# Optimization experiments

Measured on AMD Instinct MI355X. Metric: run time of the kernel, lower is better.

Reference implementation:

```python
import jax, jax.numpy as jnp
import numpy as np

D_MODEL, D_STATE, D_CONV, EXPAND = 1024, 16, 4, 2
D_INNER = EXPAND * D_MODEL
BATCH, SEQ = 2, 2048


def setup_inputs() -> dict:
    key = jax.random.key(0)
    ks = jax.random.split(key, 10)
    inv = lambda n: 1.0 / np.sqrt(n)
    return {
        "x": jax.random.normal(ks[0], (BATCH, SEQ, D_MODEL), jnp.float32),
        "in_proj_w": jax.random.uniform(ks[1], (2 * D_INNER, D_MODEL), jnp.float32, -inv(D_MODEL), inv(D_MODEL)),
        "conv_w": jax.random.uniform(ks[2], (D_INNER, D_INNER, D_CONV), jnp.float32, -inv(D_INNER * D_CONV), inv(D_INNER * D_CONV)),
        "conv_b": jax.random.uniform(ks[3], (D_INNER,), jnp.float32, -inv(D_INNER * D_CONV), inv(D_INNER * D_CONV)),
        "dt_w": jax.random.uniform(ks[4], (D_INNER, D_INNER), jnp.float32, -inv(D_INNER), inv(D_INNER)),
        "dt_b": jax.random.uniform(ks[5], (D_INNER,), jnp.float32, -inv(D_INNER), inv(D_INNER)),
        "A_log": jax.random.normal(ks[6], (D_INNER, D_STATE), jnp.float32) * 0.01,
        "D": jnp.ones((D_INNER,), jnp.float32),
        "B_w": jax.random.uniform(ks[7], (D_STATE, D_INNER), jnp.float32, -inv(D_INNER), inv(D_INNER)),
        "C_w": jax.random.uniform(ks[8], (D_STATE, D_INNER), jnp.float32, -inv(D_INNER), inv(D_INNER)),
        "out_w": jax.random.uniform(ks[9], (D_MODEL, D_INNER), jnp.float32, -inv(D_INNER), inv(D_INNER)),
    }


def _forward(x, in_proj_w, conv_w, conv_b, dt_w, dt_b, A_log, D, B_w, C_w, out_w):
    xz = x @ in_proj_w.T                      # [b, l, 2*d_inner]
    xc, z = jnp.split(xz, 2, axis=-1)
    # causal depthful conv1d (full channel mixing, left-padded)
    h = jnp.transpose(xc, (0, 2, 1))          # [b, d, l]
    h = jnp.pad(h, ((0, 0), (0, 0), (D_CONV - 1, 0)))
    h = jax.lax.conv_general_dilated(h, conv_w, (1,), 'VALID',
                                     dimension_numbers=('NCH', 'OIH', 'NCH'))
    h = h + conv_b[None, :, None]
    u = jnp.transpose(h, (0, 2, 1))           # [b, l, d_inner]

    dt = jnp.clip(jax.nn.sigmoid(u @ dt_w.T + dt_b), 1e-4, 1.0)  # [b, l, d]
    A = -jnp.exp(A_log)                       # [d, n]
    Bm = u @ B_w.T                            # [b, l, n]
    Cm = u @ C_w.T                            # [b, l, n]

    # time-major scan over the recurrence
    u_t = jnp.transpose(u, (1, 0, 2))
    dt_t = jnp.transpose(dt, (1, 0, 2))
    B_t = jnp.transpose(Bm, (1, 0, 2))
    C_t = jnp.transpose(Cm, (1, 0, 2))

    def step(state, inp):
        ut, dtt, bt, ct = inp                 # [b,d], [b,d], [b,n], [b,n]
        dA = jnp.exp(jnp.clip(dtt[:, :, None] * A, -5.0, 5.0))   # [b,d,n]
        dB = dtt[:, :, None] * bt[:, None, :] * ut[:, :, None]   # [b,d,n]
        state = dA * state + dB + 1e-6
        y = jnp.sum(state * ct[:, None, :], axis=-1) + D * ut    # [b,d]
        return state, y

    state0 = jnp.zeros((x.shape[0], D_INNER, D_STATE), x.dtype)
    _, ys = jax.lax.scan(step, state0, (u_t, dt_t, B_t, C_t))
    y = jnp.transpose(ys, (1, 0, 2))          # [b, l, d_inner]
    y = y * jax.nn.silu(z)
    return y @ out_w.T                        # [b, l, d_model]


def reference(x, in_proj_w, conv_w, conv_b, dt_w, dt_b, A_log, D, B_w, C_w, out_w):
    return _forward(x, in_proj_w, conv_w, conv_b, dt_w, dt_b, A_log, D, B_w, C_w, out_w)
```

## Files before the change

kernel.cpp:

```cpp
#include <hip/hip_runtime.h>

#define BATCHN 2
#define SEQL   2048
#define DM     1024
#define DI     2048
#define DSN    16
#define MTOT   (BATCHN * SEQL)
#define PADL   (SEQL + 3)
#define NC     64
#define CL     (SEQL / NC)
#define BCKS   8

typedef __attribute__((ext_vector_type(8))) __bf16 bf16x8;
typedef __attribute__((ext_vector_type(4))) float f32x4;

__device__ __forceinline__ unsigned short f2b(float f) {
    union { float f; unsigned u; } v; v.f = f;
    unsigned r = v.u + 0x7FFF + ((v.u >> 16) & 1);
    return (unsigned short)(r >> 16);
}
__device__ __forceinline__ float b2f(unsigned short b) {
    union { float f; unsigned u; } v; v.u = ((unsigned)b) << 16;
    return v.f;
}

__device__ __forceinline__ void gl_lds16(const void* g, void* l) {
    __builtin_amdgcn_global_load_lds(
        (const __attribute__((address_space(1))) unsigned int*)g,
        (__attribute__((address_space(3))) unsigned int*)l, 16, 0, 0);
}

__device__ __forceinline__ void swz(int& bx, int& by) {
    int gx = gridDim.x, gy = gridDim.y;
    int lin = blockIdx.y * gx + blockIdx.x;
    int xcd = lin & 7, k = lin >> 3;
    int rw = gx >> 1, rh = gy >> 2;
    by = (xcd >> 1) * rh + k / rw;
    bx = (xcd & 1) * rw + k % rw;
}

__global__ void cvt_f32_bf16(const float* __restrict__ src, unsigned short* __restrict__ dst, int n4) {
    int i = blockIdx.x * blockDim.x + threadIdx.x;
    if (i < n4) {
        float4 v = ((const float4*)src)[i];
        ushort4 o;
        o.x = f2b(v.x); o.y = f2b(v.y); o.z = f2b(v.z); o.w = f2b(v.w);
        ((ushort4*)dst)[i] = o;
    }
}

__global__ void cvt_x_pad(const float* __restrict__ src, unsigned short* __restrict__ dst) {
    int i = blockIdx.x * blockDim.x + threadIdx.x;
    if (i < MTOT * DM / 4) {
        int b = i >> 19;
        float4 v = ((const float4*)src)[i];
        ushort4 o;
        o.x = f2b(v.x); o.y = f2b(v.y); o.z = f2b(v.z); o.w = f2b(v.w);
        ((ushort4*)dst)[i + (b + 1) * (3 * DM / 4)] = o;
    }
}

__global__ void cvt_convw(const float* __restrict__ cw, unsigned short* __restrict__ wk) {
    int i = blockIdx.x * blockDim.x + threadIdx.x;
    if (i < DI * DI) {
        float4 v = ((const float4*)cw)[i];
        wk[0 * (size_t)DI * DI + i] = f2b(v.x);
        wk[1 * (size_t)DI * DI + i] = f2b(v.y);
        wk[2 * (size_t)DI * DI + i] = f2b(v.z);
        wk[3 * (size_t)DI * DI + i] = f2b(v.w);
    }
}

__global__ void __launch_bounds__(256)
tp_cvt(const float* __restrict__ src, unsigned short* __restrict__ dst) {
    __shared__ float tile[32][33];
    int ct = blockIdx.x * 32, it = blockIdx.y * 32;
    int tx = threadIdx.x & 31, ty = threadIdx.x >> 5;
#pragma unroll
    for (int r = 0; r < 4; ++r)
        tile[ty + r * 8][tx] = src[(size_t)(it + ty + r * 8) * DM + ct + tx];
    __syncthreads();
#pragma unroll
    for (int r = 0; r < 4; ++r)
        dst[(size_t)(ct + ty + r * 8) * DI + it + tx] = f2b(tile[tx][ty + r * 8]);
}

__global__ void zero_pad(unsigned short* __restrict__ xpad) {
    int i = blockIdx.x * blockDim.x + threadIdx.x;
    if (i < BATCHN * 3 * DM) {
        int b = i / (3 * DM);
        int r = i % (3 * DM);
        xpad[(size_t)b * PADL * DM + r] = 0;
    }
}

template<int MODE>
__global__ void __launch_bounds__(256)
gemm_bt(const unsigned short* __restrict__ Abase,
        const unsigned short* __restrict__ Bbase,
        const float* __restrict__ bias,
        unsigned short* __restrict__ out_bf,
        float* __restrict__ out_f,
        int K)
{
    __shared__ __align__(16) unsigned short As[128 * 64];
    __shared__ __align__(16) unsigned short Bs[128 * 64];

    const int t = threadIdx.x;
    const int lane = t & 63;
    const int wave = t >> 6;
    const int wm = wave & 1, wn = wave >> 1;
    int bx, by;
    swz(bx, by);
    const int m0 = by * 128, n0 = bx * 128;
    const int srow = t >> 3;
    const int scol = (t & 7) * 8;
    const int gcol = (((t & 7) ^ (srow & 7))) * 8;

    f32x4 acc[4][4];
#pragma unroll
    for (int i = 0; i < 4; ++i)
#pragma unroll
        for (int j = 0; j < 4; ++j)
            acc[i][j] = f32x4{0.f, 0.f, 0.f, 0.f};

    const int nseg = (MODE == 1) ? 4 : 1;
    for (int seg = 0; seg < nseg; ++seg) {
        const unsigned short* arow[4];
        const unsigned short* brow[4];
#pragma unroll
        for (int i = 0; i < 4; ++i) {
            int rg = m0 + srow + i * 32;
            if (MODE == 0) {
                arow[i] = Abase + ((size_t)(rg >> 11) * PADL + 3 + (rg & 2047)) * DM;
            } else if (MODE == 1) {
                arow[i] = Abase + ((size_t)(rg >> 11) * PADL + (rg & 2047) + seg) * DM;
            } else if (MODE == 4) {
                arow[i] = Abase + (size_t)blockIdx.z * DI * DI + (size_t)rg * K;
            } else {
                arow[i] = Abase + (size_t)rg * K;
            }
            int ng = n0 + srow + i * 32;
            if (MODE == 1)
                brow[i] = Bbase + (size_t)seg * DI * DM + (size_t)ng * DM;
            else
                brow[i] = Bbase + (size_t)ng * K;
        }
        const int Kseg = (MODE == 1) ? DM : K;
        for (int k0 = 0; k0 < Kseg; k0 += 64) {
#pragma unroll
            for (int i = 0; i < 4; ++i)
                gl_lds16(arow[i] + k0 + gcol, &As[(size_t)(srow + i * 32) * 64 + scol]);
#pragma unroll
            for (int i = 0; i < 4; ++i)
                gl_lds16(brow[i] + k0 + gcol, &Bs[(size_t)(srow + i * 32) * 64 + scol]);
            __syncthreads();
            const int qa = (lane >> 4) * 8;
            const int am = lane & 15;
            const int sw = (am & 7) << 3;
#pragma unroll
            for (int kk = 0; kk < 64; kk += 32) {
                bf16x8 af[4], bfv[4];
#pragma unroll
                for (int i = 0; i < 4; ++i)
                    af[i] = *(const bf16x8*)&As[(wm * 64 + i * 16 + am) * 64 + ((kk + qa) ^ sw)];
#pragma unroll
                for (int j = 0; j < 4; ++j)
                    bfv[j] = *(const bf16x8*)&Bs[(wn * 64 + j * 16 + am) * 64 + ((kk + qa) ^ sw)];
#pragma unroll
                for (int i = 0; i < 4; ++i)
#pragma unroll
                    for (int j = 0; j < 4; ++j)
                        acc[i][j] = __builtin_amdgcn_mfma_f32_16x16x32_bf16(
                            af[i], bfv[j], acc[i][j], 0, 0, 0);
            }
            __syncthreads();
        }
    }

    const int erow0 = m0 + wm * 64;
    const int ecol0 = n0 + wn * 64 + (lane & 15);
    const int rq = (lane >> 4) * 4;
#pragma unroll
    for (int i = 0; i < 4; ++i) {
#pragma unroll
        for (int j = 0; j < 4; ++j) {
            int col = ecol0 + j * 16;
#pragma unroll
            for (int r = 0; r < 4; ++r) {
                int row = erow0 + i * 16 + rq + r;
                float v = acc[i][j][r];
                if (MODE == 0) {
                    out_bf[(size_t)row * DI + col] = f2b(v);
                } else if (MODE == 1) {
                    v += bias[col];
                    out_bf[(size_t)row * DI + col] = f2b(v);
                } else if (MODE == 2) {
                    v += bias[col];
                    float s = 1.f / (1.f + __expf(-v));
                    s = fminf(fmaxf(s, 1e-4f), 1.f);
                    out_f[(size_t)row * DI + col] = s;
                } else if (MODE == 3) {
                    out_f[(size_t)row * DM + col] = v;
                } else {
                    out_bf[(size_t)blockIdx.z * DI * DM + (size_t)row * DM + col] = f2b(v);
                }
            }
        }
    }
}

__global__ void __launch_bounds__(256)
bc_mfma(const unsigned short* __restrict__ u,
        const unsigned short* __restrict__ w,
        float* __restrict__ pc)
{
    const int t = threadIdx.x;
    const int lane = t & 63;
    const int wave = t >> 6;
    const int ks = blockIdx.x;
    const int m0 = blockIdx.y * 128 + wave * 32;
    const int am = lane & 15, quad = lane >> 4;

    f32x4 acc[2][2];
#pragma unroll
    for (int i = 0; i < 2; ++i)
#pragma unroll
        for (int j = 0; j < 2; ++j)
            acc[i][j] = f32x4{0.f, 0.f, 0.f, 0.f};

    const int kbase = ks * (DI / BCKS);
    const unsigned short* ur0 = u + (size_t)(m0 + am) * DI;
    const unsigned short* ur1 = u + (size_t)(m0 + 16 + am) * DI;
    const unsigned short* wr0 = w + (size_t)am * DI;
    const unsigned short* wr1 = w + (size_t)(16 + am) * DI;
#pragma unroll 2
    for (int kk = 0; kk < DI / BCKS; kk += 32) {
        int k = kbase + kk + quad * 8;
        bf16x8 a0 = *(const bf16x8*)(ur0 + k);
        bf16x8 a1 = *(const bf16x8*)(ur1 + k);
        bf16x8 b0 = *(const bf16x8*)(wr0 + k);
        bf16x8 b1 = *(const bf16x8*)(wr1 + k);
        acc[0][0] = __builtin_amdgcn_mfma_f32_16x16x32_bf16(a0, b0, acc[0][0], 0, 0, 0);
        acc[0][1] = __builtin_amdgcn_mfma_f32_16x16x32_bf16(a0, b1, acc[0][1], 0, 0, 0);
        acc[1][0] = __builtin_amdgcn_mfma_f32_16x16x32_bf16(a1, b0, acc[1][0], 0, 0, 0);
        acc[1][1] = __builtin_amdgcn_mfma_f32_16x16x32_bf16(a1, b1, acc[1][1], 0, 0, 0);
    }
    float* base = pc + (size_t)ks * MTOT * 32;
#pragma unroll
    for (int i = 0; i < 2; ++i)
#pragma unroll
        for (int j = 0; j < 2; ++j)
#pragma unroll
            for (int r = 0; r < 4; ++r) {
                int row = m0 + i * 16 + quad * 4 + r;
                int col = j * 16 + am;
                base[(size_t)row * 32 + col] = acc[i][j][r];
            }
}

__global__ void __launch_bounds__(256)
bc_reduce(const float* __restrict__ pc, float* __restrict__ outf)
{
    int i = blockIdx.x * 256 + threadIdx.x;
    const float4* p4 = (const float4*)pc;
    float4 s = p4[i];
#pragma unroll
    for (int ks = 1; ks < BCKS; ++ks) {
        float4 v = p4[(size_t)ks * (MTOT * 8) + i];
        s.x += v.x; s.y += v.y; s.z += v.z; s.w += v.w;
    }
    ((float4*)outf)[i] = s;
}

__global__ void __launch_bounds__(256)
scan_p1(const float* __restrict__ dtf,
        const unsigned short* __restrict__ u_bf,
        const float* __restrict__ bcf,
        const float* __restrict__ A_log,
        float* __restrict__ Pbuf,
        float* __restrict__ Sbuf)
{
    const int t = threadIdx.x;
    const int blk = blockIdx.x;
    const int c  = blk & (NC - 1);
    const int dh = (blk >> 6) & 7;
    const int b  = blk >> 9;
    const int d  = dh * 256 + t;

    float Adn[16];
    {
        const float4* ar = (const float4*)(A_log + (size_t)d * DSN);
#pragma unroll
        for (int q = 0; q < 4; ++q) {
            float4 v = ar[q];
            Adn[q * 4 + 0] = -__expf(v.x);
            Adn[q * 4 + 1] = -__expf(v.y);
            Adn[q * 4 + 2] = -__expf(v.z);
            Adn[q * 4 + 3] = -__expf(v.w);
        }
    }
    float s[16], P[16];
#pragma unroll
    for (int n = 0; n < 16; ++n) { s[n] = 0.f; P[n] = 1.f; }

    const size_t rowbase = (size_t)b * SEQL + (size_t)c * CL;
    for (int l0 = 0; l0 < CL; l0 += 4) {
        float dt4[4], u4[4];
#pragma unroll
        for (int j = 0; j < 4; ++j) {
            size_t rb = rowbase + l0 + j;
            dt4[j] = dtf[rb * DI + d];
            u4[j] = b2f(u_bf[rb * DI + d]);
        }
#pragma unroll
        for (int j = 0; j < 4; ++j) {
            size_t rb = rowbase + l0 + j;
            const float4* Br = (const float4*)(bcf + rb * 32);
            float Bn[16];
#pragma unroll
            for (int q = 0; q < 4; ++q) {
                float4 v = Br[q];
                Bn[q * 4 + 0] = v.x; Bn[q * 4 + 1] = v.y;
                Bn[q * 4 + 2] = v.z; Bn[q * 4 + 3] = v.w;
            }
            float dt = dt4[j];
            float dBu = dt * u4[j];
#pragma unroll
            for (int n = 0; n < 16; ++n) {
                float x = dt * Adn[n];
                x = fminf(fmaxf(x, -5.f), 5.f);
                float dA = __expf(x);
                P[n] *= dA;
                s[n] = dA * s[n] + (dBu * Bn[n] + 1e-6f);
            }
        }
    }
    size_t ob = (((size_t)c * BATCHN + b) * DI + d) * DSN;
#pragma unroll
    for (int q = 0; q < 4; ++q) {
        ((float4*)(Pbuf + ob))[q] = make_float4(P[q*4], P[q*4+1], P[q*4+2], P[q*4+3]);
        ((float4*)(Sbuf + ob))[q] = make_float4(s[q*4], s[q*4+1], s[q*4+2], s[q*4+3]);
    }
}

__global__ void __launch_bounds__(256)
scan_p2(const float* __restrict__ Pbuf,
        const float* __restrict__ Sbuf,
        float* __restrict__ Ibuf)
{
    const int i = blockIdx.x * 256 + threadIdx.x;
    const int stride = BATCHN * DI * DSN;
    float s = 0.f;
    for (int c0 = 0; c0 < NC; c0 += 8) {
        float Pv[8], Sv[8];
#pragma unroll
        for (int j = 0; j < 8; ++j) {
            size_t idx = (size_t)(c0 + j) * stride + i;
            Pv[j] = Pbuf[idx];
            Sv[j] = Sbuf[idx];
        }
#pragma unroll
        for (int j = 0; j < 8; ++j) {
            size_t idx = (size_t)(c0 + j) * stride + i;
            Ibuf[idx] = s;
            s = Pv[j] * s + Sv[j];
        }
    }
}

__global__ void __launch_bounds__(256)
scan_p3(const float* __restrict__ dtf,
        const unsigned short* __restrict__ u_bf,
        const float* __restrict__ bcf,
        const unsigned short* __restrict__ z_bf,
        const float* __restrict__ A_log,
        const float* __restrict__ Dvec,
        const float* __restrict__ Ibuf,
        unsigned short* __restrict__ y_bf)
{
    const int t = threadIdx.x;
    const int blk = blockIdx.x;
    const int c  = blk & (NC - 1);
    const int dh = (blk >> 6) & 7;
    const int b  = blk >> 9;
    const int d  = dh * 256 + t;

    float Adn[16];
    {
        const float4* ar = (const float4*)(A_log + (size_t)d * DSN);
#pragma unroll
        for (int q = 0; q < 4; ++q) {
            float4 v = ar[q];
            Adn[q * 4 + 0] = -__expf(v.x);
            Adn[q * 4 + 1] = -__expf(v.y);
            Adn[q * 4 + 2] = -__expf(v.z);
            Adn[q * 4 + 3] = -__expf(v.w);
        }
    }
    const float Dd = Dvec[d];
    float s[16];
    {
        size_t ib = (((size_t)c * BATCHN + b) * DI + d) * DSN;
#pragma unroll
        for (int q = 0; q < 4; ++q) {
            float4 v = ((const float4*)(Ibuf + ib))[q];
            s[q * 4 + 0] = v.x; s[q * 4 + 1] = v.y;
            s[q * 4 + 2] = v.z; s[q * 4 + 3] = v.w;
        }
    }

    const size_t rowbase = (size_t)b * SEQL + (size_t)c * CL;
    for (int l0 = 0; l0 < CL; l0 += 4) {
        float dt4[4], u4[4], z4[4];
#pragma unroll
        for (int j = 0; j < 4; ++j) {
            size_t rb = rowbase + l0 + j;
            dt4[j] = dtf[rb * DI + d];
            u4[j] = b2f(u_bf[rb * DI + d]);
            z4[j] = b2f(z_bf[rb * DI + d]);
        }
#pragma unroll
        for (int j = 0; j < 4; ++j) {
            size_t rb = rowbase + l0 + j;
            const float4* Br = (const float4*)(bcf + rb * 32);
            float Bn[16], Cn[16];
#pragma unroll
            for (int q = 0; q < 4; ++q) {
                float4 v = Br[q];
                Bn[q * 4 + 0] = v.x; Bn[q * 4 + 1] = v.y;
                Bn[q * 4 + 2] = v.z; Bn[q * 4 + 3] = v.w;
                float4 w = Br[q + 4];
                Cn[q * 4 + 0] = w.x; Cn[q * 4 + 1] = w.y;
                Cn[q * 4 + 2] = w.z; Cn[q * 4 + 3] = w.w;
            }
            float dt = dt4[j];
            float dBu = dt * u4[j];
            float y = 0.f;
#pragma unroll
            for (int n = 0; n < 16; ++n) {
                float x = dt * Adn[n];
                x = fminf(fmaxf(x, -5.f), 5.f);
                float dA = __expf(x);
                s[n] = dA * s[n] + (dBu * Bn[n] + 1e-6f);
                y += s[n] * Cn[n];
            }
            y += Dd * u4[j];
            float zz = z4[j];
            y *= zz / (1.f + __expf(-zz));
            y_bf[rb * DI + d] = f2b(y);
        }
    }
}

extern "C" void kernel_launch(void* const* d_in, const int* in_sizes, int n_in,
                              void* d_out, int out_size, void* d_ws, size_t ws_size,
                              hipStream_t stream) {
    const float* x     = (const float*)d_in[0];
    const float* ipw   = (const float*)d_in[1];
    const float* convw = (const float*)d_in[2];
    const float* convb = (const float*)d_in[3];
    const float* dtw   = (const float*)d_in[4];
    const float* dtb   = (const float*)d_in[5];
    const float* alog  = (const float*)d_in[6];
    const float* dvec  = (const float*)d_in[7];
    const float* bw    = (const float*)d_in[8];
    const float* cwm   = (const float*)d_in[9];
    const float* ow    = (const float*)d_in[10];
    float* out = (float*)d_out;

    char* ws = (char*)d_ws;
    size_t off = 0;
    auto carve = [&](size_t bytes) {
        char* p = ws + off;
        off += (bytes + 255) & ~(size_t)255;
        return p;
    };
    unsigned short* xpad   = (unsigned short*)carve((size_t)BATCHN * PADL * DM * 2);
    unsigned short* ipz_bf = (unsigned short*)carve((size_t)DI * DM * 2);
    unsigned short* Pt_bf  = (unsigned short*)carve((size_t)DM * DI * 2);
    unsigned short* wk_bf  = (unsigned short*)carve((size_t)4 * DI * DI * 2);
    unsigned short* mk_bf  = (unsigned short*)carve((size_t)4 * DI * DM * 2);
    unsigned short* dtw_bf = (unsigned short*)carve((size_t)DI * DI * 2);
    unsigned short* ow_bf  = (unsigned short*)carve((size_t)DM * DI * 2);
    unsigned short* bc_bf  = (unsigned short*)carve((size_t)2 * DSN * DI * 2);
    unsigned short* z_bf   = (unsigned short*)carve((size_t)MTOT * DI * 2);
    unsigned short* u_bf   = (unsigned short*)carve((size_t)MTOT * DI * 2);
    float*          dt_f   = (float*)carve((size_t)MTOT * DI * 4);
    float*          bc_f   = (float*)carve((size_t)MTOT * 2 * DSN * 4);
    unsigned short* y_bf   = (unsigned short*)carve((size_t)MTOT * DI * 2);
    float*          Pbuf   = (float*)carve((size_t)NC * BATCHN * DI * DSN * 4);
    float*          Sbuf   = (float*)carve((size_t)NC * BATCHN * DI * DSN * 4);
    float*          Ibuf   = (float*)carve((size_t)NC * BATCHN * DI * DSN * 4);
    float*          pc_f   = (float*)carve((size_t)BCKS * MTOT * 32 * 4);

    cvt_x_pad<<<MTOT * DM / 4 / 256, 256, 0, stream>>>(x, xpad);
    zero_pad<<<(BATCHN * 3 * DM + 255) / 256, 256, 0, stream>>>(xpad);
    cvt_convw<<<DI * DI / 256, 256, 0, stream>>>(convw, wk_bf);
    tp_cvt<<<dim3(DM / 32, DI / 32), 256, 0, stream>>>(ipw, Pt_bf);
    cvt_f32_bf16<<<DI * DM / 4 / 256, 256, 0, stream>>>(ipw + (size_t)DI * DM, ipz_bf, DI * DM / 4);
    cvt_f32_bf16<<<DI * DI / 4 / 256, 256, 0, stream>>>(dtw, dtw_bf, DI * DI / 4);
    cvt_f32_bf16<<<DM * DI / 4 / 256, 256, 0, stream>>>(ow, ow_bf, DM * DI / 4);
    cvt_f32_bf16<<<(DSN * DI / 4 + 255) / 256, 256, 0, stream>>>(bw, bc_bf, DSN * DI / 4);
    cvt_f32_bf16<<<(DSN * DI / 4 + 255) / 256, 256, 0, stream>>>(cwm, bc_bf + (size_t)DSN * DI, DSN * DI / 4);

    gemm_bt<4><<<dim3(8, 16, 4), 256, 0, stream>>>(wk_bf, Pt_bf, nullptr, mk_bf, nullptr, DI);
    gemm_bt<0><<<dim3(16, 32), 256, 0, stream>>>(xpad, ipz_bf, nullptr, z_bf, nullptr, DM);
    gemm_bt<1><<<dim3(16, 32), 256, 0, stream>>>(xpad, mk_bf, convb, u_bf, nullptr, DM);
    bc_mfma<<<dim3(BCKS, MTOT / 128), 256, 0, stream>>>(u_bf, bc_bf, pc_f);
    bc_reduce<<<MTOT * 32 / 4 / 256, 256, 0, stream>>>(pc_f, bc_f);
    gemm_bt<2><<<dim3(16, 32), 256, 0, stream>>>(u_bf, dtw_bf, dtb, nullptr, dt_f, DI);
    scan_p1<<<BATCHN * 8 * NC, 256, 0, stream>>>(dt_f, u_bf, bc_f, alog, Pbuf, Sbuf);
    scan_p2<<<BATCHN * DI * DSN / 256, 256, 0, stream>>>(Pbuf, Sbuf, Ibuf);
    scan_p3<<<BATCHN * 8 * NC, 256, 0, stream>>>(dt_f, u_bf, bc_f, z_bf, alog, dvec, Ibuf, y_bf);
    gemm_bt<3><<<dim3(8, 32), 256, 0, stream>>>(y_bf, ow_bf, nullptr, nullptr, out, DI);
}
```

Measured before the change: 487.1 us.

## Merge conversion kernels, fuse z GEMM into conv GEMM, store dt as bf16

Combines the x-pad, zero-pad and six weight-conversion launches into two multi-role kernels, which cuts launch overhead. The z projection GEMM now runs as extra column blocks of the conv GEMM grid, so one launch replaces two and the device is better filled. The sigmoid dt output is written as bf16 instead of fp32, which halves its write traffic and the reads in both scan passes. In exchange dt loses precision, and the conv and z tiles in the merged grid do unequal work (four K segments versus one).

```diff
diff --git a/kernel.cpp b/kernel.cpp
--- a/kernel.cpp
+++ b/kernel.cpp
@@ -39,8 +39,82 @@
     bx = (xcd & 1) * rw + k % rw;
 }
 
-__global__ void cvt_f32_bf16(const float* __restrict__ src, unsigned short* __restrict__ dst, int n4) {
-    int i = blockIdx.x * blockDim.x + threadIdx.x;
+#define NB_XCVT (MTOT * DM / 4 / 256)
+__global__ void cvt_x_all(const float* __restrict__ src, unsigned short* __restrict__ dst) {
+    int blk = blockIdx.x;
+    if (blk < NB_XCVT) {
+        int i = blk * 256 + threadIdx.x;
+        int b = i >> 19;
+        float4 v = ((const float4*)src)[i];
+        ushort4 o;
+        o.x = f2b(v.x); o.y = f2b(v.y); o.z = f2b(v.z); o.w = f2b(v.w);
+        ((ushort4*)dst)[i + (b + 1) * (3 * DM / 4)] = o;
+    } else {
+        int i = (blk - NB_XCVT) * 256 + threadIdx.x;
+        if (i < BATCHN * 3 * DM) {
+            int b = i / (3 * DM);
+            int r = i % (3 * DM);
+            dst[(size_t)b * PADL * DM + r] = 0;
+        }
+    }
+}
+
+#define NB_CONVW (DI * DI / 256)
+#define NB_TP    ((DM / 32) * (DI / 32))
+#define NB_IPZ   (DI * DM / 4 / 256)
+#define NB_DTW   (DI * DI / 4 / 256)
+#define NB_OW    (DM * DI / 4 / 256)
+#define NB_BW    (DSN * DI / 4 / 256 + 1)
+__global__ void __launch_bounds__(256)
+cvt_w_all(const float* __restrict__ convw, const float* __restrict__ ipw,
+          const float* __restrict__ dtw, const float* __restrict__ ow,
+          const float* __restrict__ bw, const float* __restrict__ cw,
+          unsigned short* __restrict__ wk, unsigned short* __restrict__ Pt,
+          unsigned short* __restrict__ ipz, unsigned short* __restrict__ dtwb,
+          unsigned short* __restrict__ owb, unsigned short* __restrict__ bcb)
+{
+    __shared__ float tile[32][33];
+    int blk = blockIdx.x;
+    int t = threadIdx.x;
+    if (blk < NB_CONVW) {
+        int i = blk * 256 + t;
+        float4 v = ((const float4*)convw)[i];
+        wk[0 * (size_t)DI * DI + i] = f2b(v.x);
+        wk[1 * (size_t)DI * DI + i] = f2b(v.y);
+        wk[2 * (size_t)DI * DI + i] = f2b(v.z);
+        wk[3 * (size_t)DI * DI + i] = f2b(v.w);
+        return;
+    }
+    blk -= NB_CONVW;
+    if (blk < NB_TP) {
+        int ct = (blk & 31) * 32, it = (blk >> 5) * 32;
+        int tx = t & 31, ty = t >> 5;
+#pragma unroll
+        for (int r = 0; r < 4; ++r)
+            tile[ty + r * 8][tx] = ipw[(size_t)(it + ty + r * 8) * DM + ct + tx];
+        __syncthreads();
+#pragma unroll
+        for (int r = 0; r < 4; ++r)
+            Pt[(size_t)(ct + ty + r * 8) * DI + it + tx] = f2b(tile[tx][ty + r * 8]);
+        return;
+    }
+    blk -= NB_TP;
+    const float* src;
+    unsigned short* dst;
+    int n4;
+    if (blk < NB_IPZ) {
+        src = ipw + (size_t)DI * DM; dst = ipz; n4 = DI * DM / 4;
+    } else if ((blk -= NB_IPZ) < NB_DTW) {
+        src = dtw; dst = dtwb; n4 = DI * DI / 4;
+    } else if ((blk -= NB_DTW) < NB_OW) {
+        src = ow; dst = owb; n4 = DM * DI / 4;
+    } else if ((blk -= NB_OW) < NB_BW) {
+        src = bw; dst = bcb; n4 = DSN * DI / 4;
+    } else {
+        blk -= NB_BW;
+        src = cw; dst = bcb + (size_t)DSN * DI; n4 = DSN * DI / 4;
+    }
+    int i = blk * 256 + t;
     if (i < n4) {
         float4 v = ((const float4*)src)[i];
         ushort4 o;
@@ -49,57 +123,14 @@
     }
 }
 
-__global__ void cvt_x_pad(const float* __restrict__ src, unsigned short* __restrict__ dst) {
-    int i = blockIdx.x * blockDim.x + threadIdx.x;
-    if (i < MTOT * DM / 4) {
-        int b = i >> 19;
-        float4 v = ((const float4*)src)[i];
-        ushort4 o;
-        o.x = f2b(v.x); o.y = f2b(v.y); o.z = f2b(v.z); o.w = f2b(v.w);
-        ((ushort4*)dst)[i + (b + 1) * (3 * DM / 4)] = o;
-    }
-}
-
-__global__ void cvt_convw(const float* __restrict__ cw, unsigned short* __restrict__ wk) {
-    int i = blockIdx.x * blockDim.x + threadIdx.x;
-    if (i < DI * DI) {
-        float4 v = ((const float4*)cw)[i];
-        wk[0 * (size_t)DI * DI + i] = f2b(v.x);
-        wk[1 * (size_t)DI * DI + i] = f2b(v.y);
-        wk[2 * (size_t)DI * DI + i] = f2b(v.z);
-        wk[3 * (size_t)DI * DI + i] = f2b(v.w);
-    }
-}
-
-__global__ void __launch_bounds__(256)
-tp_cvt(const float* __restrict__ src, unsigned short* __restrict__ dst) {
-    __shared__ float tile[32][33];
-    int ct = blockIdx.x * 32, it = blockIdx.y * 32;
-    int tx = threadIdx.x & 31, ty = threadIdx.x >> 5;
-#pragma unroll
-    for (int r = 0; r < 4; ++r)
-        tile[ty + r * 8][tx] = src[(size_t)(it + ty + r * 8) * DM + ct + tx];
-    __syncthreads();
-#pragma unroll
-    for (int r = 0; r < 4; ++r)
-        dst[(size_t)(ct + ty + r * 8) * DI + it + tx] = f2b(tile[tx][ty + r * 8]);
-}
-
-__global__ void zero_pad(unsigned short* __restrict__ xpad) {
-    int i = blockIdx.x * blockDim.x + threadIdx.x;
-    if (i < BATCHN * 3 * DM) {
-        int b = i / (3 * DM);
-        int r = i % (3 * DM);
-        xpad[(size_t)b * PADL * DM + r] = 0;
-    }
-}
-
 template<int MODE>
 __global__ void __launch_bounds__(256)
 gemm_bt(const unsigned short* __restrict__ Abase,
         const unsigned short* __restrict__ Bbase,
+        const unsigned short* __restrict__ B2base,
         const float* __restrict__ bias,
         unsigned short* __restrict__ out_bf,
+        unsigned short* __restrict__ out_bf2,
         float* __restrict__ out_f,
         int K)
 {
@@ -112,7 +143,11 @@
     const int wm = wave & 1, wn = wave >> 1;
     int bx, by;
     swz(bx, by);
-    const int m0 = by * 128, n0 = bx * 128;
+    bool isz = false;
+    int n0;
+    if (MODE == 1) { isz = bx >= 16; n0 = (bx & 15) * 128; }
+    else n0 = bx * 128;
+    const int m0 = by * 128;
     const int srow = t >> 3;
     const int scol = (t & 7) * 8;
     const int gcol = (((t & 7) ^ (srow & 7))) * 8;
@@ -124,27 +159,28 @@
         for (int j = 0; j < 4; ++j)
             acc[i][j] = f32x4{0.f, 0.f, 0.f, 0.f};
 
-    const int nseg = (MODE == 1) ? 4 : 1;
+    const int nseg = (MODE == 1) ? (isz ? 1 : 4) : 1;
     for (int seg = 0; seg < nseg; ++seg) {
         const unsigned short* arow[4];
         const unsigned short* brow[4];
 #pragma unroll
         for (int i = 0; i < 4; ++i) {
             int rg = m0 + srow + i * 32;
-            if (MODE == 0) {
-                arow[i] = Abase + ((size_t)(rg >> 11) * PADL + 3 + (rg & 2047)) * DM;
-            } else if (MODE == 1) {
-                arow[i] = Abase + ((size_t)(rg >> 11) * PADL + (rg & 2047) + seg) * DM;
+            if (MODE == 1) {
+                int sh = isz ? 3 : seg;
+                arow[i] = Abase + ((size_t)(rg >> 11) * PADL + (rg & 2047) + sh) * DM;
             } else if (MODE == 4) {
                 arow[i] = Abase + (size_t)blockIdx.z * DI * DI + (size_t)rg * K;
             } else {
                 arow[i] = Abase + (size_t)rg * K;
             }
             int ng = n0 + srow + i * 32;
-            if (MODE == 1)
-                brow[i] = Bbase + (size_t)seg * DI * DM + (size_t)ng * DM;
-            else
+            if (MODE == 1) {
+                if (isz) brow[i] = B2base + (size_t)ng * DM;
+                else     brow[i] = Bbase + (size_t)seg * DI * DM + (size_t)ng * DM;
+            } else {
                 brow[i] = Bbase + (size_t)ng * K;
+            }
         }
         const int Kseg = (MODE == 1) ? DM : K;
         for (int k0 = 0; k0 < Kseg; k0 += 64) {
@@ -190,16 +226,18 @@
             for (int r = 0; r < 4; ++r) {
                 int row = erow0 + i * 16 + rq + r;
                 float v = acc[i][j][r];
-                if (MODE == 0) {
-                    out_bf[(size_t)row * DI + col] = f2b(v);
-                } else if (MODE == 1) {
-                    v += bias[col];
-                    out_bf[(size_t)row * DI + col] = f2b(v);
+                if (MODE == 1) {
+                    if (isz) {
+                        out_bf2[(size_t)row * DI + col] = f2b(v);
+                    } else {
+                        v += bias[col];
+                        out_bf[(size_t)row * DI + col] = f2b(v);
+                    }
                 } else if (MODE == 2) {
                     v += bias[col];
                     float s = 1.f / (1.f + __expf(-v));
                     s = fminf(fmaxf(s, 1e-4f), 1.f);
-                    out_f[(size_t)row * DI + col] = s;
+                    out_bf[(size_t)row * DI + col] = f2b(s);
                 } else if (MODE == 3) {
                     out_f[(size_t)row * DM + col] = v;
                 } else {
@@ -274,7 +312,7 @@
 }
 
 __global__ void __launch_bounds__(256)
-scan_p1(const float* __restrict__ dtf,
+scan_p1(const unsigned short* __restrict__ dt_bf,
         const unsigned short* __restrict__ u_bf,
         const float* __restrict__ bcf,
         const float* __restrict__ A_log,
@@ -310,7 +348,7 @@
 #pragma unroll
         for (int j = 0; j < 4; ++j) {
             size_t rb = rowbase + l0 + j;
-            dt4[j] = dtf[rb * DI + d];
+            dt4[j] = b2f(dt_bf[rb * DI + d]);
             u4[j] = b2f(u_bf[rb * DI + d]);
         }
 #pragma unroll
@@ -370,7 +408,7 @@
 }
 
 __global__ void __launch_bounds__(256)
-scan_p3(const float* __restrict__ dtf,
+scan_p3(const unsigned short* __restrict__ dt_bf,
         const unsigned short* __restrict__ u_bf,
         const float* __restrict__ bcf,
         const unsigned short* __restrict__ z_bf,
@@ -416,7 +454,7 @@
 #pragma unroll
         for (int j = 0; j < 4; ++j) {
             size_t rb = rowbase + l0 + j;
-            dt4[j] = dtf[rb * DI + d];
+            dt4[j] = b2f(dt_bf[rb * DI + d]);
             u4[j] = b2f(u_bf[rb * DI + d]);
             z4[j] = b2f(z_bf[rb * DI + d]);
         }
@@ -486,7 +524,7 @@
     unsigned short* bc_bf  = (unsigned short*)carve((size_t)2 * DSN * DI * 2);
     unsigned short* z_bf   = (unsigned short*)carve((size_t)MTOT * DI * 2);
     unsigned short* u_bf   = (unsigned short*)carve((size_t)MTOT * DI * 2);
-    float*          dt_f   = (float*)carve((size_t)MTOT * DI * 4);
+    unsigned short* dt_bf  = (unsigned short*)carve((size_t)MTOT * DI * 2);
     float*          bc_f   = (float*)carve((size_t)MTOT * 2 * DSN * 4);
     unsigned short* y_bf   = (unsigned short*)carve((size_t)MTOT * DI * 2);
     float*          Pbuf   = (float*)carve((size_t)NC * BATCHN * DI * DSN * 4);
@@ -494,24 +532,20 @@
     float*          Ibuf   = (float*)carve((size_t)NC * BATCHN * DI * DSN * 4);
     float*          pc_f   = (float*)carve((size_t)BCKS * MTOT * 32 * 4);
 
-    cvt_x_pad<<<MTOT * DM / 4 / 256, 256, 0, stream>>>(x, xpad);
-    zero_pad<<<(BATCHN * 3 * DM + 255) / 256, 256, 0, stream>>>(xpad);
-    cvt_convw<<<DI * DI / 256, 256, 0, stream>>>(convw, wk_bf);
-    tp_cvt<<<dim3(DM / 32, DI / 32), 256, 0, stream>>>(ipw, Pt_bf);
-    cvt_f32_bf16<<<DI * DM / 4 / 256, 256, 0, stream>>>(ipw + (size_t)DI * DM, ipz_bf, DI * DM / 4);
-    cvt_f32_bf16<<<DI * DI / 4 / 256, 256, 0, stream>>>(dtw, dtw_bf, DI * DI / 4);
-    cvt_f32_bf16<<<DM * DI / 4 / 256, 256, 0, stream>>>(ow, ow_bf, DM * DI / 4);
-    cvt_f32_bf16<<<(DSN * DI / 4 + 255) / 256, 256, 0, stream>>>(bw, bc_bf, DSN * DI / 4);
-    cvt_f32_bf16<<<(DSN * DI / 4 + 255) / 256, 256, 0, stream>>>(cwm, bc_bf + (size_t)DSN * DI, DSN * DI / 4);
-
-    gemm_bt<4><<<dim3(8, 16, 4), 256, 0, stream>>>(wk_bf, Pt_bf, nullptr, mk_bf, nullptr, DI);
-    gemm_bt<0><<<dim3(16, 32), 256, 0, stream>>>(xpad, ipz_bf, nullptr, z_bf, nullptr, DM);
-    gemm_bt<1><<<dim3(16, 32), 256, 0, stream>>>(xpad, mk_bf, convb, u_bf, nullptr, DM);
+    cvt_x_all<<<NB_XCVT + (BATCHN * 3 * DM + 255) / 256, 256, 0, stream>>>(x, xpad);
+    {
+        int nb = NB_CONVW + NB_TP + NB_IPZ + NB_DTW + NB_OW + 2 * NB_BW;
+        cvt_w_all<<<nb, 256, 0, stream>>>(convw, ipw, dtw, ow, bw, cwm,
+                                          wk_bf, Pt_bf, ipz_bf, dtw_bf, ow_bf, bc_bf);
+    }
+
+    gemm_bt<4><<<dim3(8, 16, 4), 256, 0, stream>>>(wk_bf, Pt_bf, nullptr, nullptr, mk_bf, nullptr, nullptr, DI);
+    gemm_bt<1><<<dim3(32, 32), 256, 0, stream>>>(xpad, mk_bf, ipz_bf, convb, u_bf, z_bf, nullptr, DM);
     bc_mfma<<<dim3(BCKS, MTOT / 128), 256, 0, stream>>>(u_bf, bc_bf, pc_f);
     bc_reduce<<<MTOT * 32 / 4 / 256, 256, 0, stream>>>(pc_f, bc_f);
-    gemm_bt<2><<<dim3(16, 32), 256, 0, stream>>>(u_bf, dtw_bf, dtb, nullptr, dt_f, DI);
-    scan_p1<<<BATCHN * 8 * NC, 256, 0, stream>>>(dt_f, u_bf, bc_f, alog, Pbuf, Sbuf);
+    gemm_bt<2><<<dim3(16, 32), 256, 0, stream>>>(u_bf, dtw_bf, nullptr, dtb, dt_bf, nullptr, nullptr, DI);
+    scan_p1<<<BATCHN * 8 * NC, 256, 0, stream>>>(dt_bf, u_bf, bc_f, alog, Pbuf, Sbuf);
     scan_p2<<<BATCHN * DI * DSN / 256, 256, 0, stream>>>(Pbuf, Sbuf, Ibuf);
-    scan_p3<<<BATCHN * 8 * NC, 256, 0, stream>>>(dt_f, u_bf, bc_f, z_bf, alog, dvec, Ibuf, y_bf);
-    gemm_bt<3><<<dim3(8, 32), 256, 0, stream>>>(y_bf, ow_bf, nullptr, nullptr, out, DI);
-}
+    scan_p3<<<BATCHN * 8 * NC, 256, 0, stream>>>(dt_bf, u_bf, bc_f, z_bf, alog, dvec, Ibuf, y_bf);
+    gemm_bt<3><<<dim3(8, 32), 256, 0, stream>>>(y_bf, ow_bf, nullptr, nullptr, nullptr, nullptr, out, DI);
+}
```

Result: slower. 559.0 us (+14.8%).
